# Optimization experiments

Hardware: AMD Instinct MI355X
Metric: run time of the kernel (lower is better)

The kernel has to match this reference:

```python
import jax, jax.numpy as jnp
import numpy as np

DIST_THRESH = 0.1
W_DIST = 0.05
W_CHAMFER = 0.05
W_SEP = 0.0005


def setup_inputs() -> dict:
    key = jax.random.key(0)
    k1, k2, k3, k4 = jax.random.split(key, 4)
    B, N, K = 4, 200000, 64
    return {
        "landmarks_C": jax.random.uniform(k1, (B, N, 3), jnp.float32),          # predicted point coords
        "landmarks_F": jax.random.normal(k2, (B, N, 4), jnp.float32) * 0.05,    # [dist, dx, dy, dz]
        "targets_C": jax.random.uniform(k3, (B, K, 3), jnp.float32),            # GT landmark coords
        "targets_F": jax.random.randint(k4, (B, K), 0, 8),                      # GT landmark class labels
        "classes": jnp.arange(6),                                               # classes to supervise
    }


def reference(landmarks_C, landmarks_F, targets_C, targets_F, classes):
    def per_batch(C_i, F_i, tC, tF):
        # class mask over GT landmarks (replaces boolean indexing in torch)
        mask_k = jnp.any(tF[None, :] == classes[:, None], axis=0)          # [K]
        n_valid = mask_k.sum()
        dists_i = F_i[:, 0]                                                # predicted distance, [N]
        coords_i = C_i + F_i[:, 1:]                                        # refined coords, [N,3]
        # pairwise dists GT landmarks -> raw point coords, invalid classes pushed to +inf
        pd = jnp.linalg.norm(C_i[None, :, :] - tC[:, None, :], axis=-1)    # [K,N]
        pd = jnp.where(mask_k[:, None], pd, jnp.inf)
        min_d = pd.min(axis=0)                                             # [N]
        pm = min_d < DIST_THRESH                                           # points near some GT landmark
        # smooth-L1 (beta=1, sum) on predicted distance; clip(inf)=2*thresh reproduces empty-target fallback
        tgt = jnp.clip(min_d, 0.0, 2.0 * DIST_THRESH)
        diff = dists_i - tgt
        ad = jnp.abs(diff)
        dist_loss = jnp.where(ad < 1.0, 0.5 * diff * diff, ad - 0.5).sum()
        # pairwise dists GT landmarks -> refined coords
        ld = jnp.linalg.norm(coords_i[None, :, :] - tC[:, None, :], axis=-1)  # [K,N]
        ld_m = jnp.where(mask_k[:, None], ld, jnp.inf)
        p2g = jnp.where(pm, ld_m.min(axis=0), 0.0)                         # pred->gt, masked points only
        g2p = jnp.where(mask_k, ld_m.min(axis=1), 0.0)                     # gt->pred, valid GT only
        chamfer = (p2g * p2g).sum() + (g2p * g2p).sum()
        # separation: ratio of dists to 2 nearest (valid) GT landmarks, per masked point
        _, idx = jax.lax.top_k(-pd.T, 2)                                   # [N,2] indices of 2 smallest
        d01 = jnp.take_along_axis(ld.T, idx, axis=1)                       # [N,2]
        sep = jnp.where(pm, d01[:, 0] / d01[:, 1], 0.0).sum()
        sep = jnp.where(n_valid >= 2, sep, 0.0)
        return W_DIST * dist_loss + W_CHAMFER * chamfer + W_SEP * sep

    losses = jax.vmap(per_batch)(landmarks_C, landmarks_F, targets_C, targets_F)
    return losses.mean()
```

## Files before the change

kernel.cpp:

```cpp
#include <hip/hip_runtime.h>


constexpr int KT = 64;
constexpr int P  = 4;
constexpr int NREP = 16;
constexpr float DIST_THRESH = 0.1f;
constexpr float W_DIST    = 0.05f;
constexpr float W_CHAMFER = 0.05f;
constexpr float W_SEP     = 0.0005f;
constexpr float PT_SENT = -1e18f;
constexpr float TG_SENT = -1e18f;
constexpr float BIGF  = 3.0e38f;
constexpr float WBIAS = 16.0f;

typedef float f2 __attribute__((ext_vector_type(2)));

__device__ __forceinline__ unsigned umin_(unsigned a, unsigned b) { return a < b ? a : b; }
__device__ __forceinline__ unsigned umax_(unsigned a, unsigned b) { return a > b ? a : b; }

__device__ __forceinline__ f2 pk_fma(f2 a, f2 b, f2 c) {
#if __has_builtin(__builtin_elementwise_fma)
    return __builtin_elementwise_fma(a, b, c);
#else
    f2 r; r.x = fmaf(a.x, b.x, c.x); r.y = fmaf(a.y, b.y, c.y); return r;
#endif
}

__global__ __launch_bounds__(128, 4)
void landmark_main(const float* __restrict__ C, const float* __restrict__ F,
                   const float* __restrict__ tC, const int* __restrict__ tF,
                   const int* __restrict__ classes, int n_classes, int N,
                   unsigned int* __restrict__ g2p_rep, float* __restrict__ sums_rep)
{
    __shared__ float4   tgtFull[KT];
    __shared__ unsigned g2pLDS[KT];
    __shared__ uint4    mK1[64], mK2[64];
    __shared__ float4   mLM[64];

    const int tid   = threadIdx.x;
    const int lane  = tid & 63;
    const int h     = tid >> 6;
    const int l31   = lane & 31;
    const int hi5   = lane >> 5;
    const int blk   = blockIdx.x;
    const int b     = blk & 3;
    const int chunk = blk >> 2;
    const int rep   = chunk & (NREP - 1);

    const float*  Cb = C + (size_t)b * N * 3;
    const float4* Fb = (const float4*)(F + (size_t)b * N * 4);
    const int base = chunk * (64 * P);

    float4 rf[P]; float rX[P], rY[P], rZ[P];
    #pragma unroll
    for (int p = 0; p < P; ++p) {
        int n = base + p * 64 + lane;
        int ni = (n < N) ? n : 0;
        rf[p] = Fb[ni];
        rX[p] = Cb[3 * ni + 0];
        rY[p] = Cb[3 * ni + 1];
        rZ[p] = Cb[3 * ni + 2];
    }

    if (tid < KT) {
        int f = tF[b * KT + tid];
        float x = tC[(b * KT + tid) * 3 + 0];
        float y = tC[(b * KT + tid) * 3 + 1];
        float z = tC[(b * KT + tid) * 3 + 2];
        bool valid = false;
        for (int c = 0; c < n_classes; ++c) valid = valid || (f == classes[c]);
        if (!valid) { x = TG_SENT; y = TG_SENT; z = TG_SENT; }
        tgtFull[tid] = make_float4(-2.f * x, -2.f * y, -2.f * z,
                                   x * x + y * y + z * z + WBIAS);
        g2pLDS[tid] = 0x7F7FFFFFu;
    }
    __syncthreads();

    f2 pcx[P], pcy[P], pcz[P];
    float ppm[P], ccm[P], f0[P];
    #pragma unroll
    for (int p = 0; p < P; ++p) {
        int n = base + p * 64 + lane;
        bool v = (n < N);
        float4 f4 = rf[p];
        float X = rX[p], Y = rY[p], Z = rZ[p];
        f0[p] = v ? f4.x : 2.0f * DIST_THRESH;
        if (!v) { X = PT_SENT; Y = PT_SENT; Z = PT_SENT; f4.y = f4.z = f4.w = 0.f; }
        float cxv = X + f4.y, cyv = Y + f4.z, czv = Z + f4.w;
        pcx[p] = (f2){X, cxv};
        pcy[p] = (f2){Y, cyv};
        pcz[p] = (f2){Z, czv};
        ppm[p] = fmaf(Z, Z, fmaf(Y, Y, X * X)) - WBIAS;
        ccm[p] = fmaf(czv, czv, fmaf(cyv, cyv, cxv * cxv)) - WBIAS;
    }

    unsigned k1[P], k2[P];
    float lmin[P];
    #pragma unroll
    for (int p = 0; p < P; ++p) { k1[p] = 0xFFFFFFFFu; k2[p] = 0xFFFFFFFFu; lmin[p] = BIGF; }

    const unsigned tkb = (unsigned)((l31 ^ (hi5 << 4)) | (h << 5));

    float4 Tb[2][4];
    #pragma unroll
    for (int j = 0; j < 4; ++j) Tb[0][j] = tgtFull[tkb ^ (unsigned)j];

    #pragma unroll
    for (int g = 0; g < 8; ++g) {
        const int cur = g & 1, nxt = cur ^ 1;
        if (g < 7) {
            #pragma unroll
            for (int j = 0; j < 4; ++j)
                Tb[nxt][j] = tgtFull[tkb ^ (unsigned)((g + 1) * 4 + j)];
        }
        #pragma unroll
        for (int j = 0; j < 4; ++j) {
            const unsigned tk = tkb ^ (unsigned)(g * 4 + j);
            const float4 T = Tb[cur][j];
            const f2 Tx = {T.x, T.x}, Ty = {T.y, T.y}, Tz = {T.z, T.z}, Tw = {T.w, T.w};
            float av[P];
            #pragma unroll
            for (int p = 0; p < P; ++p) {
                f2 w2 = pk_fma(pcx[p], Tx, pk_fma(pcy[p], Ty, pk_fma(pcz[p], Tz, Tw)));
                unsigned key = (__float_as_uint(w2.x) & 0xFFFFFFC0u) | tk;
                unsigned hi = umax_(k1[p], key);
                k1[p] = umin_(k1[p], key);
                k2[p] = umin_(k2[p], hi);
                lmin[p] = fminf(lmin[p], w2.y);
                av[p] = w2.y + ccm[p];
            }
            float dl = fmaxf(fminf(fminf(av[0], av[1]), fminf(av[2], av[3])), 0.f);
            atomicMin(&g2pLDS[tk], __float_as_uint(dl));
        }
    }

    if (h == 0) {
        mK1[lane] = make_uint4(k1[0], k1[1], k1[2], k1[3]);
        mK2[lane] = make_uint4(k2[0], k2[1], k2[2], k2[3]);
        mLM[lane] = make_float4(lmin[0], lmin[1], lmin[2], lmin[3]);
    }
    __syncthreads();

    if (h == 0) {
        atomicMax(&g2p_rep[rep * 256 + b * 64 + lane], ~g2pLDS[lane]);
    } else {
        uint4 A1 = mK1[lane], A2 = mK2[lane];
        float4 AL = mLM[lane];
        const unsigned a1v[P] = {A1.x, A1.y, A1.z, A1.w};
        const unsigned a2v[P] = {A2.x, A2.y, A2.z, A2.w};
        const float    alv[P] = {AL.x, AL.y, AL.z, AL.w};

        float dist_acc = 0.f, p2g_acc = 0.f, sep_acc = 0.f;
        #pragma unroll
        for (int p = 0; p < P; ++p) {
            unsigned m1 = umin_(a1v[p], k1[p]);
            unsigned m2 = umin_(umax_(a1v[p], k1[p]), umin_(a2v[p], k2[p]));
            float lm = fminf(alv[p], lmin[p]);
            float keyf1 = __uint_as_float(m1 & 0xFFFFFFC0u);
            float mind = sqrtf(fmaxf(keyf1 + ppm[p], 0.f));
            bool pm = mind < DIST_THRESH;
            float tgtv = fminf(mind, 2.0f * DIST_THRESH);
            float diff = f0[p] - tgtv;
            float ad = fabsf(diff);
            dist_acc += (ad < 1.0f) ? 0.5f * diff * diff : (ad - 0.5f);
            if (pm) {
                p2g_acc += fmaxf(lm + ccm[p], 0.f);
                int i1 = (int)(m1 & 63u), i2 = (int)(m2 & 63u);
                float4 T1 = tgtFull[i1], T2 = tgtFull[i2];
                float cxv = pcx[p].y, cyv = pcy[p].y, czv = pcz[p].y;
                float l1sq = fmaf(cxv, T1.x, fmaf(cyv, T1.y, fmaf(czv, T1.z, T1.w))) + ccm[p];
                float l2sq = fmaf(cxv, T2.x, fmaf(cyv, T2.y, fmaf(czv, T2.z, T2.w))) + ccm[p];
                sep_acc += sqrtf(fmaxf(l1sq, 0.f) / fmaxf(l2sq, 1e-30f));
            }
        }

        float v0 = dist_acc, v1 = p2g_acc, v2 = sep_acc;
        #pragma unroll
        for (int o = 32; o > 0; o >>= 1) {
            v0 += __shfl_down(v0, o, 64);
            v1 += __shfl_down(v1, o, 64);
            v2 += __shfl_down(v2, o, 64);
        }
        if (lane == 0) {
            float* sb = sums_rep + rep * 16 + b;
            atomicAdd(sb + 0, v0);
            atomicAdd(sb + 4, v1);
            atomicAdd(sb + 8, v2);
        }
    }
}

__global__ void landmark_finalize(const int* __restrict__ tF, const int* __restrict__ classes,
                                  int n_classes, const unsigned int* __restrict__ g2p_rep,
                                  const float* __restrict__ sums_rep, float* __restrict__ out)
{
    __shared__ float lossb[4];
    const int tid = threadIdx.x;
    const int b = tid >> 6, k = tid & 63;

    int f = tF[b * KT + k];
    bool valid = false;
    for (int c = 0; c < n_classes; ++c) valid = valid || (f == classes[c]);

    unsigned enc = 0;
    for (int r = 0; r < NREP; ++r) enc = umax_(enc, g2p_rep[r * 256 + b * 64 + k]);
    float g  = valid ? __uint_as_float(~enc) : 0.f;
    float nv = valid ? 1.f : 0.f;

    #pragma unroll
    for (int o = 32; o > 0; o >>= 1) {
        g  += __shfl_down(g, o, 64);
        nv += __shfl_down(nv, o, 64);
    }
    if (k == 0) {
        float sd = 0.f, sp = 0.f, ss = 0.f;
        for (int r = 0; r < NREP; ++r) {
            sd += sums_rep[r * 16 + 0 + b];
            sp += sums_rep[r * 16 + 4 + b];
            ss += sums_rep[r * 16 + 8 + b];
        }
        float sep = (nv >= 2.f) ? ss : 0.f;
        lossb[b] = W_DIST * sd + W_CHAMFER * (sp + g) + W_SEP * sep;
    }
    __syncthreads();
    if (tid == 0)
        out[0] = (lossb[0] + lossb[1] + lossb[2] + lossb[3]) * 0.25f;
}

extern "C" void kernel_launch(void* const* d_in, const int* in_sizes, int n_in,
                              void* d_out, int out_size, void* d_ws, size_t ws_size,
                              hipStream_t stream)
{
    const float* C       = (const float*)d_in[0];
    const float* F       = (const float*)d_in[1];
    const float* tC      = (const float*)d_in[2];
    const int*   tF      = (const int*)d_in[3];
    const int*   classes = (const int*)d_in[4];
    const int n_classes = in_sizes[4];
    const int B = 4;
    const int N = in_sizes[0] / (3 * B);

    unsigned int* g2p_rep  = (unsigned int*)d_ws;
    float*        sums_rep = (float*)((char*)d_ws + NREP * 256 * 4);

    hipMemsetAsync(d_ws, 0, NREP * 256 * 4 + NREP * 16 * 4, stream);

    const int cpb = (N + 64 * P - 1) / (64 * P);
    landmark_main<<<cpb * 4, 128, 0, stream>>>(C, F, tC, tF, classes, n_classes,
                                               N, g2p_rep, sums_rep);
    landmark_finalize<<<1, 256, 0, stream>>>(tF, classes, n_classes, g2p_rep,
                                             sums_rep, (float*)d_out);
}
```

Measured before the change: 97.21 us.

## Broadcast targets via readlane and reduce gt-to-pred minima with DPP

Each wave now keeps its 32 target records in registers and broadcasts them to all lanes with readlane, instead of reading swizzled float4s from LDS. The per-target LDS atomicMin for the gt-to-pred minimum is replaced by a DPP wave-level min reduction plus a readlane, and each lane keeps the result for its own target. This removes the LDS accumulator, its initialisation and the first block barrier. In exchange, every target step now runs a serial chain of about a dozen DPP/min instructions plus readlanes, which adds ALU work and latency to the inner loop.

```diff
diff --git a/kernel.cpp b/kernel.cpp
--- a/kernel.cpp
+++ b/kernel.cpp
@@ -26,6 +26,17 @@
 #endif
 }
 
+__device__ __forceinline__ unsigned dpp_umin64(unsigned v) {
+    unsigned t;
+    t = (unsigned)__builtin_amdgcn_update_dpp(0x7F7FFFFF, (int)v, 0x111, 0xF, 0xF, false); v = umin_(v, t);
+    t = (unsigned)__builtin_amdgcn_update_dpp(0x7F7FFFFF, (int)v, 0x112, 0xF, 0xF, false); v = umin_(v, t);
+    t = (unsigned)__builtin_amdgcn_update_dpp(0x7F7FFFFF, (int)v, 0x114, 0xF, 0xF, false); v = umin_(v, t);
+    t = (unsigned)__builtin_amdgcn_update_dpp(0x7F7FFFFF, (int)v, 0x118, 0xF, 0xF, false); v = umin_(v, t);
+    t = (unsigned)__builtin_amdgcn_update_dpp(0x7F7FFFFF, (int)v, 0x142, 0xF, 0xF, false); v = umin_(v, t);
+    t = (unsigned)__builtin_amdgcn_update_dpp(0x7F7FFFFF, (int)v, 0x143, 0xF, 0xF, false); v = umin_(v, t);
+    return v;
+}
+
 __global__ __launch_bounds__(128, 4)
 void landmark_main(const float* __restrict__ C, const float* __restrict__ F,
                    const float* __restrict__ tC, const int* __restrict__ tF,
@@ -33,7 +44,6 @@
                    unsigned int* __restrict__ g2p_rep, float* __restrict__ sums_rep)
 {
     __shared__ float4   tgtFull[KT];
-    __shared__ unsigned g2pLDS[KT];
     __shared__ uint4    mK1[64], mK2[64];
     __shared__ float4   mLM[64];
 
@@ -62,19 +72,21 @@
         rZ[p] = Cb[3 * ni + 2];
     }
 
-    if (tid < KT) {
-        int f = tF[b * KT + tid];
-        float x = tC[(b * KT + tid) * 3 + 0];
-        float y = tC[(b * KT + tid) * 3 + 1];
-        float z = tC[(b * KT + tid) * 3 + 2];
-        bool valid = false;
-        for (int c = 0; c < n_classes; ++c) valid = valid || (f == classes[c]);
-        if (!valid) { x = TG_SENT; y = TG_SENT; z = TG_SENT; }
-        tgtFull[tid] = make_float4(-2.f * x, -2.f * y, -2.f * z,
-                                   x * x + y * y + z * z + WBIAS);
-        g2pLDS[tid] = 0x7F7FFFFFu;
-    }
-    __syncthreads();
+    const int tgt = (h << 5) | l31;
+    int   tfv = tF[b * KT + tgt];
+    float tx = tC[(b * KT + tgt) * 3 + 0];
+    float ty = tC[(b * KT + tgt) * 3 + 1];
+    float tz = tC[(b * KT + tgt) * 3 + 2];
+    bool tvalid = false;
+    for (int c = 0; c < n_classes; ++c) tvalid = tvalid || (tfv == classes[c]);
+    if (!tvalid) { tx = TG_SENT; ty = TG_SENT; tz = TG_SENT; }
+    const float4 vT = make_float4(-2.f * tx, -2.f * ty, -2.f * tz,
+                                  tx * tx + ty * ty + tz * tz + WBIAS);
+    if (hi5 == 0) tgtFull[tgt] = vT;
+    const unsigned tbx = __float_as_uint(vT.x);
+    const unsigned tby = __float_as_uint(vT.y);
+    const unsigned tbz = __float_as_uint(vT.z);
+    const unsigned tbw = __float_as_uint(vT.w);
 
     f2 pcx[P], pcy[P], pcz[P];
     float ppm[P], ccm[P], f0[P];
@@ -99,40 +111,36 @@
     #pragma unroll
     for (int p = 0; p < P; ++p) { k1[p] = 0xFFFFFFFFu; k2[p] = 0xFFFFFFFFu; lmin[p] = BIGF; }
 
-    const unsigned tkb = (unsigned)((l31 ^ (hi5 << 4)) | (h << 5));
-
-    float4 Tb[2][4];
-    #pragma unroll
-    for (int j = 0; j < 4; ++j) Tb[0][j] = tgtFull[tkb ^ (unsigned)j];
-
-    #pragma unroll
-    for (int g = 0; g < 8; ++g) {
-        const int cur = g & 1, nxt = cur ^ 1;
-        if (g < 7) {
-            #pragma unroll
-            for (int j = 0; j < 4; ++j)
-                Tb[nxt][j] = tgtFull[tkb ^ (unsigned)((g + 1) * 4 + j)];
-        }
+    unsigned g2pacc = 0x7F7FFFFFu;
+    const unsigned hb = (unsigned)(h << 5);
+
+    #pragma unroll 8
+    for (int i = 0; i < 32; ++i) {
+        const float Txs = __uint_as_float((unsigned)__builtin_amdgcn_readlane((int)tbx, i));
+        const float Tys = __uint_as_float((unsigned)__builtin_amdgcn_readlane((int)tby, i));
+        const float Tzs = __uint_as_float((unsigned)__builtin_amdgcn_readlane((int)tbz, i));
+        const float Tws = __uint_as_float((unsigned)__builtin_amdgcn_readlane((int)tbw, i));
+        const unsigned tk = (unsigned)i | hb;
+        const f2 Tx = {Txs, Txs}, Ty = {Tys, Tys}, Tz = {Tzs, Tzs}, Tw = {Tws, Tws};
+        float av[P];
         #pragma unroll
-        for (int j = 0; j < 4; ++j) {
-            const unsigned tk = tkb ^ (unsigned)(g * 4 + j);
-            const float4 T = Tb[cur][j];
-            const f2 Tx = {T.x, T.x}, Ty = {T.y, T.y}, Tz = {T.z, T.z}, Tw = {T.w, T.w};
-            float av[P];
-            #pragma unroll
-            for (int p = 0; p < P; ++p) {
-                f2 w2 = pk_fma(pcx[p], Tx, pk_fma(pcy[p], Ty, pk_fma(pcz[p], Tz, Tw)));
-                unsigned key = (__float_as_uint(w2.x) & 0xFFFFFFC0u) | tk;
-                unsigned hi = umax_(k1[p], key);
-                k1[p] = umin_(k1[p], key);
-                k2[p] = umin_(k2[p], hi);
-                lmin[p] = fminf(lmin[p], w2.y);
-                av[p] = w2.y + ccm[p];
-            }
-            float dl = fmaxf(fminf(fminf(av[0], av[1]), fminf(av[2], av[3])), 0.f);
-            atomicMin(&g2pLDS[tk], __float_as_uint(dl));
-        }
-    }
+        for (int p = 0; p < P; ++p) {
+            f2 w2 = pk_fma(pcx[p], Tx, pk_fma(pcy[p], Ty, pk_fma(pcz[p], Tz, Tw)));
+            unsigned key = (__float_as_uint(w2.x) & 0xFFFFFFC0u) | tk;
+            unsigned hi = umax_(k1[p], key);
+            k1[p] = umin_(k1[p], key);
+            k2[p] = umin_(k2[p], hi);
+            lmin[p] = fminf(lmin[p], w2.y);
+            av[p] = w2.y + ccm[p];
+        }
+        float dl = fmaxf(fminf(fminf(av[0], av[1]), fminf(av[2], av[3])), 0.f);
+        unsigned red = dpp_umin64(__float_as_uint(dl));
+        unsigned rs = (unsigned)__builtin_amdgcn_readlane((int)red, 63);
+        g2pacc = (l31 == i) ? rs : g2pacc;
+    }
+
+    if (hi5 == 0)
+        atomicMax(&g2p_rep[rep * 256 + b * 64 + tgt], ~g2pacc);
 
     if (h == 0) {
         mK1[lane] = make_uint4(k1[0], k1[1], k1[2], k1[3]);
@@ -141,9 +149,7 @@
     }
     __syncthreads();
 
-    if (h == 0) {
-        atomicMax(&g2p_rep[rep * 256 + b * 64 + lane], ~g2pLDS[lane]);
-    } else {
+    if (h == 1) {
         uint4 A1 = mK1[lane], A2 = mK2[lane];
         float4 AL = mLM[lane];
         const unsigned a1v[P] = {A1.x, A1.y, A1.z, A1.w};
@@ -243,7 +249,7 @@
     unsigned int* g2p_rep  = (unsigned int*)d_ws;
     float*        sums_rep = (float*)((char*)d_ws + NREP * 256 * 4);
 
-    hipMemsetAsync(d_ws, 0, NREP * 256 * 4 + NREP * 16 * 4, stream);
+    (void)hipMemsetAsync(d_ws, 0, NREP * 256 * 4 + NREP * 16 * 4, stream);
 
     const int cpb = (N + 64 * P - 1) / (64 * P);
     landmark_main<<<cpb * 4, 128, 0, stream>>>(C, F, tC, tF, classes, n_classes,
```

Result: slower. 106.5 us (+9.6%).
